# Performance work log

Hardware: AMD Instinct MI355X
Metric: run time of the kernel (lower is better)

Reference implementation:

```python
import jax, jax.numpy as jnp
import numpy as np
import math

N_EMBD = 768
N_HEAD = 12
B, T, S = 8, 1024, 257
HEAD_DIM = N_EMBD // N_HEAD


def _ln(x, g, b, eps=1e-5):
    m = jnp.mean(x, axis=-1, keepdims=True)
    v = jnp.mean(jnp.square(x - m), axis=-1, keepdims=True)
    return (x - m) * jax.lax.rsqrt(v + eps) * g + b


def _heads(t, n_head):
    b, s, c = t.shape
    return t.reshape(b, s, n_head, c // n_head).transpose(0, 2, 1, 3)  # (B,H,S,D)


def setup_inputs() -> dict:
    key = jax.random.key(0)
    ks = jax.random.split(key, 12)
    sc = 0.02
    d, h4 = N_EMBD, 4 * N_EMBD
    return {
        "x": jax.random.normal(ks[0], (B, T, d), jnp.float32),
        "encoder_x": jax.random.normal(ks[1], (B, S, d), jnp.float32),
        "ln1_g": jnp.ones((d,), jnp.float32), "ln1_b": jnp.zeros((d,), jnp.float32),
        "ln2_g": jnp.ones((d,), jnp.float32), "ln2_b": jnp.zeros((d,), jnp.float32),
        "ln3_g": jnp.ones((d,), jnp.float32), "ln3_b": jnp.zeros((d,), jnp.float32),
        "attn_w": jax.random.normal(ks[2], (d, 3 * d), jnp.float32) * sc,
        "attn_b": jnp.zeros((3 * d,), jnp.float32),
        "attn_proj_w": jax.random.normal(ks[3], (d, d), jnp.float32) * sc,
        "attn_proj_b": jnp.zeros((d,), jnp.float32),
        "cross_w": jax.random.normal(ks[4], (d, 3 * d), jnp.float32) * sc,
        "cross_b": jnp.zeros((3 * d,), jnp.float32),
        "cross_proj_w": jax.random.normal(ks[5], (d, d), jnp.float32) * sc,
        "cross_proj_b": jnp.zeros((d,), jnp.float32),
        "fc_w": jax.random.normal(ks[6], (d, h4), jnp.float32) * sc,
        "fc_b": jnp.zeros((h4,), jnp.float32),
        "proj_w": jax.random.normal(ks[7], (h4, d), jnp.float32) * sc,
        "proj_b": jnp.zeros((d,), jnp.float32),
    }


def reference(x, encoder_x, ln1_g, ln1_b, ln2_g, ln2_b, ln3_g, ln3_b,
              attn_w, attn_b, attn_proj_w, attn_proj_b,
              cross_w, cross_b, cross_proj_w, cross_proj_b,
              fc_w, fc_b, proj_w, proj_b):
    d = N_EMBD
    scale = 1.0 / math.sqrt(HEAD_DIM)

    # --- causal self-attention ---
    h = _ln(x, ln1_g, ln1_b)
    qkv = h @ attn_w + attn_b
    q, k, v = (_heads(t, N_HEAD) for t in jnp.split(qkv, 3, axis=-1))
    att = jnp.einsum('bhqd,bhkd->bhqk', q, k) * scale
    t = x.shape[1]
    causal = jnp.tril(jnp.ones((t, t), bool))
    att = jnp.where(causal[None, None], att, -jnp.inf)
    att = jax.nn.softmax(att, axis=-1)
    o = jnp.einsum('bhqk,bhkd->bhqd', att, v)
    o = o.transpose(0, 2, 1, 3).reshape(x.shape)
    x = x + o @ attn_proj_w + attn_proj_b

    # --- cross-attention (shared c_attn for q from x, k/v from encoder) ---
    h = _ln(x, ln2_g, ln2_b)
    q = _heads((h @ cross_w + cross_b)[..., :d], N_HEAD)
    ekv = encoder_x @ cross_w + cross_b
    k = _heads(ekv[..., d:2 * d], N_HEAD)
    v = _heads(ekv[..., 2 * d:], N_HEAD)
    att = jax.nn.softmax(jnp.einsum('bhqd,bhkd->bhqk', q, k) * scale, axis=-1)
    o = jnp.einsum('bhqk,bhkd->bhqd', att, v)
    o = o.transpose(0, 2, 1, 3).reshape(x.shape)
    x = x + o @ cross_proj_w + cross_proj_b

    # --- MLP (GELU tanh) ---
    h = _ln(x, ln3_g, ln3_b)
    h = jax.nn.gelu(h @ fc_w + fc_b, approximate=True)
    x = x + h @ proj_w + proj_b
    return x
```

## Files before the change

kernel.cpp:

```cpp
#include <hip/hip_runtime.h>

typedef __bf16 bf16x8 __attribute__((ext_vector_type(8)));
typedef float  f32x4  __attribute__((ext_vector_type(4)));
typedef unsigned short u16;

#define N_EMBD 768
#define T_LEN 1024
#define S_LEN 257
#define S_PAD 320
#define BATCH 8
#define NH 12
#define BH (BATCH*NH)
#define HD 64

__device__ __forceinline__ u16 f2b(float f){
  union{float f; unsigned u;} v; v.f=f;
  unsigned r=(v.u + 0x7fffu + ((v.u>>16)&1u))>>16;
  return (u16)r;
}
__device__ __forceinline__ float b2f(u16 h){
  union{unsigned u; float f;} v; v.u=((unsigned)h)<<16;
  return v.f;
}
__device__ __forceinline__ void gl_lds16(const void* g, void* l){
  __builtin_amdgcn_global_load_lds((const __attribute__((address_space(1))) void*)g,
                                   (__attribute__((address_space(3))) void*)l, 16, 0, 0);
}

template<int C> __device__ __forceinline__ float dpp_mov_f(float x){
  union{float f;int i;} u; u.f=x;
  u.i = __builtin_amdgcn_mov_dpp(u.i, C, 0xf, 0xf, true);
  return u.f;
}
__device__ __forceinline__ float red16_add(float x){
  x = x + dpp_mov_f<0xB1>(x);
  x = x + dpp_mov_f<0x4E>(x);
  x = x + dpp_mov_f<0x141>(x);
  x = x + dpp_mov_f<0x140>(x);
  return x;
}

__global__ void cvt_f32_bf16(const float* __restrict__ in, u16* __restrict__ out, int n4){
  int i = blockIdx.x*256 + threadIdx.x;
  if(i < n4){
    float4 f = *(const float4*)&in[i*4];
    ushort4 u; u.x=f2b(f.x); u.y=f2b(f.y); u.z=f2b(f.z); u.w=f2b(f.w);
    *(ushort4*)&out[i*4] = u;
  }
}

__global__ void transpose_all(const float* __restrict__ s0,const float* __restrict__ s1,
                              const float* __restrict__ s2,const float* __restrict__ s3,
                              const float* __restrict__ s4,const float* __restrict__ s5,
                              u16* __restrict__ d0,u16* __restrict__ d1,
                              u16* __restrict__ d2,u16* __restrict__ d3,
                              u16* __restrict__ d4,u16* __restrict__ d5){
  __shared__ u16 tile[64][68];
  int id=blockIdx.x;
  const float* in; u16* out; int K,N,t;
  if(id<432)      {in=s0;out=d0;K=768;N=2304;t=id;}
  else if(id<864) {in=s1;out=d1;K=768;N=2304;t=id-432;}
  else if(id<1008){in=s2;out=d2;K=768;N=768;t=id-864;}
  else if(id<1152){in=s3;out=d3;K=768;N=768;t=id-1008;}
  else if(id<1728){in=s4;out=d4;K=768;N=3072;t=id-1152;}
  else            {in=s5;out=d5;K=3072;N=768;t=id-1728;}
  int tiles_n=N>>6;
  int k0=(t/tiles_n)<<6, n0=(t%tiles_n)<<6;
  int tr = threadIdx.x>>4;
  int tc = (threadIdx.x&15)*4;
#pragma unroll
  for(int i=0;i<4;i++){
    float4 f = *(const float4*)&in[(size_t)(k0+tr+i*16)*N + n0 + tc];
    tile[tr+i*16][tc+0]=f2b(f.x); tile[tr+i*16][tc+1]=f2b(f.y);
    tile[tr+i*16][tc+2]=f2b(f.z); tile[tr+i*16][tc+3]=f2b(f.w);
  }
  __syncthreads();
#pragma unroll
  for(int i=0;i<4;i++){
    int n = n0+tr+i*16;
    ushort4 u;
    u.x=tile[tc+0][tr+i*16]; u.y=tile[tc+1][tr+i*16];
    u.z=tile[tc+2][tr+i*16]; u.w=tile[tc+3][tr+i*16];
    *(ushort4*)&out[(size_t)n*K + k0 + tc] = u;
  }
}

__global__ void ln_kernel(const float* __restrict__ x, const float* __restrict__ g,
                          const float* __restrict__ bta, u16* __restrict__ out){
  int row  = blockIdx.x*4 + (threadIdx.x>>6);
  int lane = threadIdx.x&63;
  size_t base = (size_t)row*N_EMBD;
  float v[12];
#pragma unroll
  for(int p=0;p<3;p++){
    int col = p*256 + lane*4;
    float4 f = *(const float4*)&x[base+col];
    v[p*4]=f.x; v[p*4+1]=f.y; v[p*4+2]=f.z; v[p*4+3]=f.w;
  }
  float s=0.f, s2=0.f;
#pragma unroll
  for(int i=0;i<12;i++){ s+=v[i]; s2+=v[i]*v[i]; }
#pragma unroll
  for(int off=1; off<64; off<<=1){ s += __shfl_xor(s,off); s2 += __shfl_xor(s2,off); }
  float mean = s*(1.f/N_EMBD);
  float var  = s2*(1.f/N_EMBD) - mean*mean;
  float rstd = rsqrtf(var + 1e-5f);
#pragma unroll
  for(int p=0;p<3;p++){
    int col = p*256 + lane*4;
#pragma unroll
    for(int j=0;j<4;j++){
      out[base+col+j] = f2b((v[p*4+j]-mean)*rstd*g[col+j] + bta[col+j]);
    }
  }
}

enum { M_QKV_SELF=0, M_Q_CROSS=1, M_KV_CROSS=2, M_RESID_F32=3,
       M_RESID_INPLACE=4, M_GELU=5, M_RESID_OUT=6 };

template<int MODE, int BN>
__global__ void gemm_bt(const u16* __restrict__ A, const u16* __restrict__ Wt,
                        const float* __restrict__ bias,
                        void* out0, void* out1, void* out2, const void* resid,
                        int M, int K, int Ntiles){
  constexpr int MI = (BN==128)?4:2;
  __shared__ u16 As[128*64];
  __shared__ u16 Bs[BN*64];
  int tid=threadIdx.x, wave=tid>>6, lane=tid&63;

  int Mtl = gridDim.x / Ntiles;
  int mt, nt;
  if((Mtl&7)==0){
    int xcd=blockIdx.x&7, j=blockIdx.x>>3, bpx=Mtl>>3;
    int band=j/Ntiles; nt=j-band*Ntiles; mt=xcd*bpx+band;
  } else { mt=blockIdx.x/Ntiles; nt=blockIdx.x-mt*Ntiles; }
  int m0=mt*128, n0=nt*BN;

  int wm = (BN==128)? (wave>>1)*64 : wave*32;
  int wn = (BN==128)? (wave&1)*64  : 0;
  int lrow=lane&15, quad=lane>>4;
  f32x4 acc[MI][4];
  f32x4 z = {0.f,0.f,0.f,0.f};
#pragma unroll
  for(int i=0;i<MI;i++)
#pragma unroll
    for(int j=0;j<4;j++) acc[i][j]=z;

  int srow  = wave*8 + (lane>>3);
  int c_src = (lane&7) ^ ((lane>>3)&7);
  int pa = quad ^ (lrow&7);

  for(int k0=0;k0<K;k0+=64){
#pragma unroll
    for(int i=0;i<4;i++){
      int row = i*32 + srow;
      int ga = min(m0+row, M-1);
      gl_lds16(A + (size_t)ga*K + k0 + c_src*8, &As[(i*32+wave*8)*64]);
    }
#pragma unroll
    for(int i=0;i<BN/32;i++){
      int row = i*32 + srow;
      gl_lds16(Wt + (size_t)(n0+row)*K + k0 + c_src*8, &Bs[(i*32+wave*8)*64]);
    }
    __syncthreads();
    bf16x8 af[MI][2], bfr[4][2];
#pragma unroll
    for(int i=0;i<MI;i++){
      const u16* ab=&As[(wm+i*16+lrow)*64];
      af[i][0]=*(const bf16x8*)(ab+pa*8);
      af[i][1]=*(const bf16x8*)(ab+(pa^4)*8);
    }
#pragma unroll
    for(int i=0;i<4;i++){
      const u16* bb=&Bs[(wn+i*16+lrow)*64];
      bfr[i][0]=*(const bf16x8*)(bb+pa*8);
      bfr[i][1]=*(const bf16x8*)(bb+(pa^4)*8);
    }
#pragma unroll
    for(int h=0;h<2;h++)
#pragma unroll
      for(int mi=0;mi<MI;mi++)
#pragma unroll
        for(int ni=0;ni<4;ni++)
          acc[mi][ni] = __builtin_amdgcn_mfma_f32_16x16x32_bf16(af[mi][h], bfr[ni][h], acc[mi][ni], 0,0,0);
    __syncthreads();
  }

#pragma unroll
  for(int ni=0;ni<4;ni++){
    int n = n0 + wn + ni*16 + lrow;
    float bv = bias[n];
#pragma unroll
    for(int mi=0;mi<MI;mi++){
      int mbase = m0 + wm + mi*16 + quad*4;
      float cr[4];
#pragma unroll
      for(int r=0;r<4;r++) cr[r]=acc[mi][ni][r]+bv;

      if constexpr (MODE==M_QKV_SELF){
        int part=n/768, nn=n-part*768;
        int hh=nn>>6, dd=nn&63;
        int b=mbase>>10, t0=mbase&1023;
        size_t bh=(size_t)(b*NH+hh);
        if(part==0){
#pragma unroll
          for(int r=0;r<4;r++) ((u16*)out0)[(bh*T_LEN+t0+r)*HD+dd]=f2b(cr[r]*0.125f);
        } else if(part==1){
#pragma unroll
          for(int r=0;r<4;r++) ((u16*)out1)[(bh*T_LEN+t0+r)*HD+dd]=f2b(cr[r]);
        } else {
          ushort4 pk; pk.x=f2b(cr[0]); pk.y=f2b(cr[1]); pk.z=f2b(cr[2]); pk.w=f2b(cr[3]);
          *(ushort4*)&((u16*)out2)[(bh*HD+dd)*T_LEN+t0]=pk;
        }
      } else if constexpr (MODE==M_Q_CROSS){
        int b=mbase>>10, t0=mbase&1023;
        int hh=n>>6, dd=n&63;
        size_t bh=(size_t)(b*NH+hh);
#pragma unroll
        for(int r=0;r<4;r++) ((u16*)out0)[(bh*T_LEN+t0+r)*HD+dd]=f2b(cr[r]*0.125f);
      } else if constexpr (MODE==M_KV_CROSS){
        int part=n/768, nn=n-part*768;
        int hh=nn>>6, dd=nn&63;
#pragma unroll
        for(int r=0;r<4;r++){
          int m=mbase+r;
          if(m<M){
            int b=m/S_LEN, s=m-b*S_LEN;
            size_t bh=(size_t)(b*NH+hh);
            if(part==0) ((u16*)out0)[(bh*S_PAD+s)*HD+dd]=f2b(cr[r]);
            else        ((u16*)out1)[(bh*HD+dd)*S_PAD+s]=f2b(cr[r]);
          }
        }
      } else if constexpr (MODE==M_RESID_F32){
        const float* x=(const float*)resid;
#pragma unroll
        for(int r=0;r<4;r++){ int m=mbase+r;
          ((float*)out0)[(size_t)m*768+n]=x[(size_t)m*768+n]+cr[r]; }
      } else if constexpr (MODE==M_RESID_INPLACE){
#pragma unroll
        for(int r=0;r<4;r++){ int m=mbase+r;
          ((float*)out0)[(size_t)m*768+n]+=cr[r]; }
      } else if constexpr (MODE==M_GELU){
#pragma unroll
        for(int r=0;r<4;r++){
          int m=mbase+r;
          float uu=cr[r];
          float zz=0.7978845608028654f*(uu+0.044715f*uu*uu*uu);
          float t=__expf(2.f*zz);
          float th=1.f-2.f/(t+1.f);
          ((u16*)out0)[(size_t)m*3072+n]=f2b(0.5f*uu*(1.f+th));
        }
      } else {
        const float* x=(const float*)resid;
#pragma unroll
        for(int r=0;r<4;r++){ int m=mbase+r;
          ((float*)out0)[(size_t)m*768+n]=x[(size_t)m*768+n]+cr[r]; }
      }
    }
  }
}

template<bool CAUSAL>
__global__ __launch_bounds__(256,2)
void flash_attn(const u16* __restrict__ Q, const u16* __restrict__ Kk,
                const u16* __restrict__ V, u16* __restrict__ O,
                int Skey, int Spad){
  __shared__ u16 KT[2][64*64];
  __shared__ u16 VT[2][64*64];
  __shared__ u16 Plds[4][16][72];
  int bh = blockIdx.x % BH;
  int qbi= blockIdx.x / BH;
  int qb = CAUSAL ? (15-qbi) : qbi;
  int b=bh/NH, hh=bh-b*NH;
  int wave=threadIdx.x>>6, lane=threadIdx.x&63;
  int lrow=lane&15, quad=lane>>4;
  const u16* Qp=Q+(size_t)bh*T_LEN*HD;
  const u16* Kp=Kk+(size_t)bh*Spad*HD;
  const u16* Vp=V+(size_t)bh*HD*Spad;
  u16* Op=O+(size_t)b*T_LEN*N_EMBD+hh*HD;
  int q0 = qb*64 + wave*16;

  int r0    = wave*8 + (lane>>3);
  int c_src = (lane&7) ^ ((lane>>3)&7);

  bf16x8 aq0=*(const bf16x8*)&Qp[(size_t)(q0+lrow)*HD + quad*8];
  bf16x8 aq1=*(const bf16x8*)&Qp[(size_t)(q0+lrow)*HD + 32 + quad*8];

  f32x4 oacc[4];
  f32x4 z={0.f,0.f,0.f,0.f};
#pragma unroll
  for(int i=0;i<4;i++) oacc[i]=z;
  float lsum[4]={0.f,0.f,0.f,0.f};

  int nt = CAUSAL ? (qb+1) : ((Skey+63)>>6);

  {
    gl_lds16(Kp + (size_t)r0*HD        + c_src*8, &KT[0][(wave*8)*64]);
    gl_lds16(Kp + (size_t)(r0+32)*HD   + c_src*8, &KT[0][(32+wave*8)*64]);
    gl_lds16(Vp + (size_t)r0*Spad      + c_src*8, &VT[0][(wave*8)*64]);
    gl_lds16(Vp + (size_t)(r0+32)*Spad + c_src*8, &VT[0][(32+wave*8)*64]);
  }
  __syncthreads();

  int p0 = quad ^ (lrow&7);

  for(int it=0; it<nt; it++){
    int bb = it&1;
    int kt = it*64;
    if(it+1<nt){
      int ktn=(it+1)*64;
      gl_lds16(Kp + (size_t)(ktn+r0)*HD      + c_src*8, &KT[bb^1][(wave*8)*64]);
      gl_lds16(Kp + (size_t)(ktn+r0+32)*HD   + c_src*8, &KT[bb^1][(32+wave*8)*64]);
      gl_lds16(Vp + (size_t)r0*Spad      + ktn + c_src*8, &VT[bb^1][(wave*8)*64]);
      gl_lds16(Vp + (size_t)(r0+32)*Spad + ktn + c_src*8, &VT[bb^1][(32+wave*8)*64]);
    }
    f32x4 s[4];
#pragma unroll
    for(int g=0;g<4;g++){
      const u16* kb=&KT[bb][(g*16+lrow)*64];
      bf16x8 bk0=*(const bf16x8*)(kb+p0*8);
      bf16x8 bk1=*(const bf16x8*)(kb+(p0^4)*8);
      s[g]=z;
      s[g]=__builtin_amdgcn_mfma_f32_16x16x32_bf16(aq0,bk0,s[g],0,0,0);
      s[g]=__builtin_amdgcn_mfma_f32_16x16x32_bf16(aq1,bk1,s[g],0,0,0);
    }
    bool domask = (it==nt-1);
#pragma unroll
    for(int r=0;r<4;r++){
      float sv0=s[0][r], sv1=s[1][r], sv2=s[2][r], sv3=s[3][r];
      if(domask){
        if(CAUSAL){
          int q=q0+quad*4+r;
          if(kt+lrow    >q) sv0=-3.0e38f;
          if(kt+16+lrow >q) sv1=-3.0e38f;
          if(kt+32+lrow >q) sv2=-3.0e38f;
          if(kt+48+lrow >q) sv3=-3.0e38f;
        } else {
          if(kt+lrow    >=Skey) sv0=-3.0e38f;
          if(kt+16+lrow >=Skey) sv1=-3.0e38f;
          if(kt+32+lrow >=Skey) sv2=-3.0e38f;
          if(kt+48+lrow >=Skey) sv3=-3.0e38f;
        }
      }
      float p0e=__expf(sv0), p1e=__expf(sv1);
      float p2e=__expf(sv2), p3e=__expf(sv3);
      lsum[r] += (p0e+p1e)+(p2e+p3e);
      Plds[wave][quad*4+r][lrow]    = f2b(p0e);
      Plds[wave][quad*4+r][16+lrow] = f2b(p1e);
      Plds[wave][quad*4+r][32+lrow] = f2b(p2e);
      Plds[wave][quad*4+r][48+lrow] = f2b(p3e);
    }
    bf16x8 ap0=*(const bf16x8*)&Plds[wave][lrow][quad*8];
    bf16x8 ap1=*(const bf16x8*)&Plds[wave][lrow][32+quad*8];
#pragma unroll
    for(int dt=0;dt<4;dt++){
      const u16* vb=&VT[bb][(dt*16+lrow)*64];
      bf16x8 bv0=*(const bf16x8*)(vb+p0*8);
      bf16x8 bv1=*(const bf16x8*)(vb+(p0^4)*8);
      oacc[dt]=__builtin_amdgcn_mfma_f32_16x16x32_bf16(ap0,bv0,oacc[dt],0,0,0);
      oacc[dt]=__builtin_amdgcn_mfma_f32_16x16x32_bf16(ap1,bv1,oacc[dt],0,0,0);
    }
    __syncthreads();
  }
  float linv[4];
#pragma unroll
  for(int r=0;r<4;r++) linv[r]=1.f/red16_add(lsum[r]);
#pragma unroll
  for(int dt=0;dt<4;dt++){
#pragma unroll
    for(int r=0;r<4;r++){
      int q=q0+quad*4+r;
      Op[(size_t)q*N_EMBD + dt*16 + lrow]=f2b(oacc[dt][r]*linv[r]);
    }
  }
}

extern "C" void kernel_launch(void* const* d_in, const int* in_sizes, int n_in,
                              void* d_out, int out_size, void* d_ws, size_t ws_size,
                              hipStream_t stream){
  const float* x_in   =(const float*)d_in[0];
  const float* enc    =(const float*)d_in[1];
  const float* ln1_g  =(const float*)d_in[2];
  const float* ln1_b  =(const float*)d_in[3];
  const float* ln2_g  =(const float*)d_in[4];
  const float* ln2_b  =(const float*)d_in[5];
  const float* ln3_g  =(const float*)d_in[6];
  const float* ln3_b  =(const float*)d_in[7];
  const float* attn_w =(const float*)d_in[8];
  const float* attn_b =(const float*)d_in[9];
  const float* attn_pw=(const float*)d_in[10];
  const float* attn_pb=(const float*)d_in[11];
  const float* cross_w=(const float*)d_in[12];
  const float* cross_b=(const float*)d_in[13];
  const float* cross_pw=(const float*)d_in[14];
  const float* cross_pb=(const float*)d_in[15];
  const float* fc_w   =(const float*)d_in[16];
  const float* fc_b   =(const float*)d_in[17];
  const float* proj_w =(const float*)d_in[18];
  const float* proj_b =(const float*)d_in[19];

  char* ws=(char*)d_ws;
  u16*  attn_wT  =(u16*)(ws + 0);
  u16*  cross_wT =(u16*)(ws + 3538944);
  u16*  attn_pwT =(u16*)(ws + 7077888);
  u16*  cross_pwT=(u16*)(ws + 8257536);
  u16*  fc_wT    =(u16*)(ws + 9437184);
  u16*  proj_wT  =(u16*)(ws + 14155776);
  float* xcur    =(float*)(ws + 18874368);
  u16*  hbuf     =(u16*)(ws + 44040192);
  u16*  Qs       =(u16*)(ws + 56623104);
  u16*  Ks       =(u16*)(ws + 69206016);
  u16*  Vst      =(u16*)(ws + 81788928);
  u16*  Qc       =(u16*)(ws + 94371840);
  u16*  hf       =(u16*)(ws + 56623104);
  u16*  Kc       =(u16*)(ws + 106954752);
  u16*  Vct      =(u16*)(ws + 110886912);
  u16*  enc_bf   =(u16*)(ws + 114819072);

  dim3 blk(256);
  cvt_f32_bf16<<<1542,blk,0,stream>>>(enc, enc_bf, 394752);
  transpose_all<<<2304,blk,0,stream>>>(attn_w, cross_w, attn_pw, cross_pw, fc_w, proj_w,
                                       attn_wT, cross_wT, attn_pwT, cross_pwT, fc_wT, proj_wT);

  ln_kernel<<<2048,blk,0,stream>>>(x_in, ln1_g, ln1_b, hbuf);
  gemm_bt<M_QKV_SELF,128><<<1152,blk,0,stream>>>(hbuf, attn_wT, attn_b,
      Qs, Ks, Vst, nullptr, 8192, 768, 18);
  flash_attn<true><<<1536,blk,0,stream>>>(Qs, Ks, Vst, hbuf, 1024, 1024);
  gemm_bt<M_RESID_F32,64><<<768,blk,0,stream>>>(hbuf, attn_pwT, attn_pb,
      xcur, nullptr, nullptr, x_in, 8192, 768, 12);

  ln_kernel<<<2048,blk,0,stream>>>(xcur, ln2_g, ln2_b, hbuf);
  gemm_bt<M_Q_CROSS,64><<<768,blk,0,stream>>>(hbuf, cross_wT, cross_b,
      Qc, nullptr, nullptr, nullptr, 8192, 768, 12);
  gemm_bt<M_KV_CROSS,64><<<408,blk,0,stream>>>(enc_bf, cross_wT + 768*768,
      cross_b + 768, Kc, Vct, nullptr, nullptr, 2056, 768, 24);
  flash_attn<false><<<1536,blk,0,stream>>>(Qc, Kc, Vct, hbuf, S_LEN, S_PAD);
  gemm_bt<M_RESID_INPLACE,64><<<768,blk,0,stream>>>(hbuf, cross_pwT, cross_pb,
      xcur, nullptr, nullptr, nullptr, 8192, 768, 12);

  ln_kernel<<<2048,blk,0,stream>>>(xcur, ln3_g, ln3_b, hbuf);
  gemm_bt<M_GELU,128><<<1536,blk,0,stream>>>(hbuf, fc_wT, fc_b,
      hf, nullptr, nullptr, nullptr, 8192, 768, 24);
  gemm_bt<M_RESID_OUT,64><<<768,blk,0,stream>>>(hf, proj_wT, proj_b,
      d_out, nullptr, nullptr, xcur, 8192, 3072, 12);
}
```

Measured before the change: 436.8 us.

## Add 256x256-tile 8-wave GEMM for QKV and FC projections

Introduces a new GEMM kernel with 256x256 output tiles, 512 threads, and double-buffered LDS staging. The A and B half-tiles are loaded in an interleaved, ping-pong schedule, with s_setprio around the MFMA blocks and XCD-aware tile mapping. It replaces the 128-tile GEMM for the self-attention QKV projection and the MLP fc+GELU projection. The aim is more data reuse per block and better overlap of global loads with MFMA work. In exchange, grids are smaller (288 and 384 blocks, so a partial wave on 256 CUs), register pressure is high, and there are many barriers.

```diff
diff --git a/kernel.cpp b/kernel.cpp
--- a/kernel.cpp
+++ b/kernel.cpp
@@ -258,6 +258,193 @@
       }
     }
   }
+}
+
+template<int MODE>
+__global__ __launch_bounds__(512)
+void gemm256(const u16* __restrict__ A, const u16* __restrict__ Wt,
+             const float* __restrict__ bias,
+             void* out0, void* out1, void* out2,
+             int K, int Ntl){
+  __shared__ u16 Asl[2][256*64];
+  __shared__ u16 Bsl[2][256*64];
+  int tid=threadIdx.x, wave=tid>>6, lane=tid&63;
+  int wr=wave>>2, wn=wave&3;
+  int lrow=lane&15, quad=lane>>4;
+
+  int Mtl = gridDim.x / Ntl;
+  int mt, ntb;
+  if((Mtl&7)==0){
+    int xcd=blockIdx.x&7, j=blockIdx.x>>3, bpx=Mtl>>3;
+    int band=j/Ntl; ntb=j-band*Ntl; mt=xcd*bpx+band;
+  } else { mt=blockIdx.x/Ntl; ntb=blockIdx.x-mt*Ntl; }
+  int m0=mt*256, n0=ntb*256;
+
+  int srow8  = lane>>3;
+  int scsrc  = (lane&7) ^ (srow8&7);
+  int pa     = quad ^ (lrow&7);
+
+  float bv[4];
+#pragma unroll
+  for(int ni=0;ni<4;ni++) bv[ni]=bias[n0 + wn*64 + ni*16 + lrow];
+
+  f32x4 acc[8][4];
+  f32x4 z={0.f,0.f,0.f,0.f};
+#pragma unroll
+  for(int i=0;i<8;i++)
+#pragma unroll
+    for(int j=0;j<4;j++) acc[i][j]=z;
+
+  const int NT = K>>6;
+
+#define STG(mat, baser, u, half, lsl) do{                                     \
+    const u16* _g = (mat) + ((size_t)((baser)+(half)*128))*(size_t)K + (size_t)(u)*64; \
+    u16* _l = &lsl[(u)&1][(half)*128*64];                                     \
+    _Pragma("unroll")                                                         \
+    for(int _j=0;_j<2;_j++){                                                  \
+      int _rr = _j*64 + wave*8 + srow8;                                       \
+      gl_lds16(_g + (size_t)_rr*K + scsrc*8, _l + (_j*64+wave*8)*64);         \
+    }                                                                         \
+  }while(0)
+#define MEMFENCE() asm volatile("" ::: "memory")
+#define BAR() __builtin_amdgcn_s_barrier()
+
+  STG(A,  m0, 0, 0, Asl); STG(A,  m0, 0, 1, Asl);
+  STG(Wt, n0, 0, 0, Bsl); STG(Wt, n0, 0, 1, Bsl);
+  STG(A,  m0, 1, 0, Asl); STG(A,  m0, 1, 1, Asl);
+  asm volatile("s_waitcnt vmcnt(4)" ::: "memory");
+  BAR();
+  MEMFENCE();
+
+  bf16x8 a[8][2], b[4][2];
+
+  for(int t=0;t<NT;t++){
+    int s=t&1;
+    const u16* as=&Asl[s][0];
+    const u16* bs=&Bsl[s][0];
+
+#pragma unroll
+    for(int mi=0;mi<4;mi++){
+      const u16* p=&as[(wr*128+mi*16+lrow)*64];
+      a[mi][0]=*(const bf16x8*)(p+pa*8);
+      a[mi][1]=*(const bf16x8*)(p+(pa^4)*8);
+    }
+#pragma unroll
+    for(int ni=0;ni<2;ni++){
+      const u16* p=&bs[(wn*64+ni*16+lrow)*64];
+      b[ni][0]=*(const bf16x8*)(p+pa*8);
+      b[ni][1]=*(const bf16x8*)(p+(pa^4)*8);
+    }
+    if(t+1<NT) STG(Wt, n0, t+1, 0, Bsl);
+    MEMFENCE(); BAR(); MEMFENCE();
+    __builtin_amdgcn_s_setprio(1);
+#pragma unroll
+    for(int mi=0;mi<4;mi++)
+#pragma unroll
+      for(int ni=0;ni<2;ni++){
+        acc[mi][ni]=__builtin_amdgcn_mfma_f32_16x16x32_bf16(a[mi][0],b[ni][0],acc[mi][ni],0,0,0);
+        acc[mi][ni]=__builtin_amdgcn_mfma_f32_16x16x32_bf16(a[mi][1],b[ni][1],acc[mi][ni],0,0,0);
+      }
+    __builtin_amdgcn_s_setprio(0);
+    MEMFENCE(); BAR(); MEMFENCE();
+
+#pragma unroll
+    for(int mi=4;mi<8;mi++){
+      const u16* p=&as[(wr*128+mi*16+lrow)*64];
+      a[mi][0]=*(const bf16x8*)(p+pa*8);
+      a[mi][1]=*(const bf16x8*)(p+(pa^4)*8);
+    }
+    if(t+1<NT) STG(Wt, n0, t+1, 1, Bsl);
+    MEMFENCE(); BAR(); MEMFENCE();
+    __builtin_amdgcn_s_setprio(1);
+#pragma unroll
+    for(int mi=4;mi<8;mi++)
+#pragma unroll
+      for(int ni=0;ni<2;ni++){
+        acc[mi][ni]=__builtin_amdgcn_mfma_f32_16x16x32_bf16(a[mi][0],b[ni][0],acc[mi][ni],0,0,0);
+        acc[mi][ni]=__builtin_amdgcn_mfma_f32_16x16x32_bf16(a[mi][1],b[ni][1],acc[mi][ni],0,0,0);
+      }
+    __builtin_amdgcn_s_setprio(0);
+    MEMFENCE(); BAR(); MEMFENCE();
+
+#pragma unroll
+    for(int ni=2;ni<4;ni++){
+      const u16* p=&bs[(wn*64+ni*16+lrow)*64];
+      b[ni][0]=*(const bf16x8*)(p+pa*8);
+      b[ni][1]=*(const bf16x8*)(p+(pa^4)*8);
+    }
+    if(t+2<NT) STG(A, m0, t+2, 0, Asl);
+    MEMFENCE(); BAR(); MEMFENCE();
+    __builtin_amdgcn_s_setprio(1);
+#pragma unroll
+    for(int mi=0;mi<4;mi++)
+#pragma unroll
+      for(int ni=2;ni<4;ni++){
+        acc[mi][ni]=__builtin_amdgcn_mfma_f32_16x16x32_bf16(a[mi][0],b[ni][0],acc[mi][ni],0,0,0);
+        acc[mi][ni]=__builtin_amdgcn_mfma_f32_16x16x32_bf16(a[mi][1],b[ni][1],acc[mi][ni],0,0,0);
+      }
+    __builtin_amdgcn_s_setprio(0);
+    MEMFENCE(); BAR(); MEMFENCE();
+
+    if(t+2<NT) STG(A, m0, t+2, 1, Asl);
+    MEMFENCE(); BAR(); MEMFENCE();
+    __builtin_amdgcn_s_setprio(1);
+#pragma unroll
+    for(int mi=4;mi<8;mi++)
+#pragma unroll
+      for(int ni=2;ni<4;ni++){
+        acc[mi][ni]=__builtin_amdgcn_mfma_f32_16x16x32_bf16(a[mi][0],b[ni][0],acc[mi][ni],0,0,0);
+        acc[mi][ni]=__builtin_amdgcn_mfma_f32_16x16x32_bf16(a[mi][1],b[ni][1],acc[mi][ni],0,0,0);
+      }
+    __builtin_amdgcn_s_setprio(0);
+    if(t+2<NT){
+      asm volatile("s_waitcnt vmcnt(4)" ::: "memory");
+    } else if(t+1<NT){
+      asm volatile("s_waitcnt vmcnt(0)" ::: "memory");
+    }
+    MEMFENCE(); BAR(); MEMFENCE();
+  }
+#undef STG
+
+#pragma unroll
+  for(int ni=0;ni<4;ni++){
+    int n = n0 + wn*64 + ni*16 + lrow;
+#pragma unroll
+    for(int mi=0;mi<8;mi++){
+      int mbase = m0 + wr*128 + mi*16 + quad*4;
+      float cr[4];
+#pragma unroll
+      for(int r=0;r<4;r++) cr[r]=acc[mi][ni][r]+bv[ni];
+
+      if constexpr (MODE==M_QKV_SELF){
+        int part=n/768, nn=n-part*768;
+        int hh=nn>>6, dd=nn&63;
+        int b_=mbase>>10, t0=mbase&1023;
+        size_t bh=(size_t)(b_*NH+hh);
+        if(part==0){
+#pragma unroll
+          for(int r=0;r<4;r++) ((u16*)out0)[(bh*T_LEN+t0+r)*HD+dd]=f2b(cr[r]*0.125f);
+        } else if(part==1){
+#pragma unroll
+          for(int r=0;r<4;r++) ((u16*)out1)[(bh*T_LEN+t0+r)*HD+dd]=f2b(cr[r]);
+        } else {
+          ushort4 pk; pk.x=f2b(cr[0]); pk.y=f2b(cr[1]); pk.z=f2b(cr[2]); pk.w=f2b(cr[3]);
+          *(ushort4*)&((u16*)out2)[(bh*HD+dd)*T_LEN+t0]=pk;
+        }
+      } else if constexpr (MODE==M_GELU){
+#pragma unroll
+        for(int r=0;r<4;r++){
+          int m=mbase+r;
+          float uu=cr[r];
+          float zz=0.7978845608028654f*(uu+0.044715f*uu*uu*uu);
+          float tt=__expf(2.f*zz);
+          float th=1.f-2.f/(tt+1.f);
+          ((u16*)out0)[(size_t)m*3072+n]=f2b(0.5f*uu*(1.f+th));
+        }
+      }
+    }
+  }
+  (void)out1; (void)out2;
 }
 
 template<bool CAUSAL>
@@ -423,8 +610,8 @@
                                        attn_wT, cross_wT, attn_pwT, cross_pwT, fc_wT, proj_wT);
 
   ln_kernel<<<2048,blk,0,stream>>>(x_in, ln1_g, ln1_b, hbuf);
-  gemm_bt<M_QKV_SELF,128><<<1152,blk,0,stream>>>(hbuf, attn_wT, attn_b,
-      Qs, Ks, Vst, nullptr, 8192, 768, 18);
+  gemm256<M_QKV_SELF><<<288,dim3(512),0,stream>>>(hbuf, attn_wT, attn_b,
+      Qs, Ks, Vst, 768, 9);
   flash_attn<true><<<1536,blk,0,stream>>>(Qs, Ks, Vst, hbuf, 1024, 1024);
   gemm_bt<M_RESID_F32,64><<<768,blk,0,stream>>>(hbuf, attn_pwT, attn_pb,
       xcur, nullptr, nullptr, x_in, 8192, 768, 12);
@@ -439,8 +626,8 @@
       xcur, nullptr, nullptr, nullptr, 8192, 768, 12);
 
   ln_kernel<<<2048,blk,0,stream>>>(xcur, ln3_g, ln3_b, hbuf);
-  gemm_bt<M_GELU,128><<<1536,blk,0,stream>>>(hbuf, fc_wT, fc_b,
-      hf, nullptr, nullptr, nullptr, 8192, 768, 24);
+  gemm256<M_GELU><<<384,dim3(512),0,stream>>>(hbuf, fc_wT, fc_b,
+      hf, nullptr, nullptr, 768, 12);
   gemm_bt<M_RESID_OUT,64><<<768,blk,0,stream>>>(hf, proj_wT, proj_b,
       d_out, nullptr, nullptr, xcur, 8192, 3072, 12);
 }
```

Measured after the change: 486.4 us. +11.4%, slower.

## Double-buffer GEMM LDS tiles and widen N-tiles for projection GEMMs

Applied to the files above, without the earlier changes.

Shared-memory tiles in the GEMM kernel are now double-buffered, so the global-to-LDS copy for the next K-step is issued before the MFMA work on the current buffer. This removes one barrier per step and lets memory loads overlap with matrix math. The projection, cross-Q and output GEMMs also switch from 64-wide to 128-wide N tiles, halving grid size and increasing reuse of the A tile. The cost is twice the LDS per block and fewer blocks, which can lower occupancy and leave the 256 CUs less evenly loaded with 384 blocks.

```diff
diff --git a/kernel.cpp b/kernel.cpp
--- a/kernel.cpp
+++ b/kernel.cpp
@@ -118,14 +118,51 @@
 enum { M_QKV_SELF=0, M_Q_CROSS=1, M_KV_CROSS=2, M_RESID_F32=3,
        M_RESID_INPLACE=4, M_GELU=5, M_RESID_OUT=6 };
 
+#define GB_STAGE(k0v, BUF) do{                                                \
+    _Pragma("unroll")                                                         \
+    for(int i_=0;i_<4;i_++){                                                  \
+      int row_=i_*32+srow;                                                    \
+      int ga_=min(m0+row_, M-1);                                              \
+      gl_lds16(A + (size_t)ga_*K + (k0v) + c_src*8, &As[BUF][(i_*32+wave*8)*64]); \
+    }                                                                         \
+    _Pragma("unroll")                                                         \
+    for(int i_=0;i_<BN/32;i_++){                                              \
+      int row_=i_*32+srow;                                                    \
+      gl_lds16(Wt + (size_t)(n0+row_)*K + (k0v) + c_src*8, &Bs[BUF][(i_*32+wave*8)*64]); \
+    }                                                                         \
+  }while(0)
+
+#define GB_COMPUTE(BUF) do{                                                   \
+    bf16x8 af[MI][2], bfr[4][2];                                              \
+    _Pragma("unroll")                                                         \
+    for(int i_=0;i_<MI;i_++){                                                 \
+      const u16* ab_=&As[BUF][(wm+i_*16+lrow)*64];                            \
+      af[i_][0]=*(const bf16x8*)(ab_+pa*8);                                   \
+      af[i_][1]=*(const bf16x8*)(ab_+(pa^4)*8);                               \
+    }                                                                         \
+    _Pragma("unroll")                                                         \
+    for(int i_=0;i_<4;i_++){                                                  \
+      const u16* bb_=&Bs[BUF][(wn+i_*16+lrow)*64];                            \
+      bfr[i_][0]=*(const bf16x8*)(bb_+pa*8);                                  \
+      bfr[i_][1]=*(const bf16x8*)(bb_+(pa^4)*8);                              \
+    }                                                                         \
+    _Pragma("unroll")                                                         \
+    for(int h_=0;h_<2;h_++)                                                   \
+      _Pragma("unroll")                                                       \
+      for(int mi_=0;mi_<MI;mi_++)                                             \
+        _Pragma("unroll")                                                     \
+        for(int ni_=0;ni_<4;ni_++)                                            \
+          acc[mi_][ni_]=__builtin_amdgcn_mfma_f32_16x16x32_bf16(af[mi_][h_],bfr[ni_][h_],acc[mi_][ni_],0,0,0); \
+  }while(0)
+
 template<int MODE, int BN>
 __global__ void gemm_bt(const u16* __restrict__ A, const u16* __restrict__ Wt,
                         const float* __restrict__ bias,
                         void* out0, void* out1, void* out2, const void* resid,
                         int M, int K, int Ntiles){
   constexpr int MI = (BN==128)?4:2;
-  __shared__ u16 As[128*64];
-  __shared__ u16 Bs[BN*64];
+  __shared__ u16 As[2][128*64];
+  __shared__ u16 Bs[2][BN*64];
   int tid=threadIdx.x, wave=tid>>6, lane=tid&63;
 
   int Mtl = gridDim.x / Ntiles;
@@ -150,40 +187,21 @@
   int c_src = (lane&7) ^ ((lane>>3)&7);
   int pa = quad ^ (lrow&7);
 
-  for(int k0=0;k0<K;k0+=64){
-#pragma unroll
-    for(int i=0;i<4;i++){
-      int row = i*32 + srow;
-      int ga = min(m0+row, M-1);
-      gl_lds16(A + (size_t)ga*K + k0 + c_src*8, &As[(i*32+wave*8)*64]);
-    }
-#pragma unroll
-    for(int i=0;i<BN/32;i++){
-      int row = i*32 + srow;
-      gl_lds16(Wt + (size_t)(n0+row)*K + k0 + c_src*8, &Bs[(i*32+wave*8)*64]);
-    }
+  const int NT = K>>6;
+  GB_STAGE(0, 0);
+  __syncthreads();
+
+  for(int t=0;t<NT;t+=2){
+    if(t+1<NT) GB_STAGE((t+1)*64, 1);
+    __builtin_amdgcn_sched_barrier(0);
+    GB_COMPUTE(0);
     __syncthreads();
-    bf16x8 af[MI][2], bfr[4][2];
-#pragma unroll
-    for(int i=0;i<MI;i++){
-      const u16* ab=&As[(wm+i*16+lrow)*64];
-      af[i][0]=*(const bf16x8*)(ab+pa*8);
-      af[i][1]=*(const bf16x8*)(ab+(pa^4)*8);
-    }
-#pragma unroll
-    for(int i=0;i<4;i++){
-      const u16* bb=&Bs[(wn+i*16+lrow)*64];
-      bfr[i][0]=*(const bf16x8*)(bb+pa*8);
-      bfr[i][1]=*(const bf16x8*)(bb+(pa^4)*8);
-    }
-#pragma unroll
-    for(int h=0;h<2;h++)
-#pragma unroll
-      for(int mi=0;mi<MI;mi++)
-#pragma unroll
-        for(int ni=0;ni<4;ni++)
-          acc[mi][ni] = __builtin_amdgcn_mfma_f32_16x16x32_bf16(af[mi][h], bfr[ni][h], acc[mi][ni], 0,0,0);
-    __syncthreads();
+    if(t+1<NT){
+      if(t+2<NT) GB_STAGE((t+2)*64, 0);
+      __builtin_amdgcn_sched_barrier(0);
+      GB_COMPUTE(1);
+      __syncthreads();
+    }
   }
 
 #pragma unroll
@@ -426,21 +444,21 @@
   gemm_bt<M_QKV_SELF,128><<<1152,blk,0,stream>>>(hbuf, attn_wT, attn_b,
       Qs, Ks, Vst, nullptr, 8192, 768, 18);
   flash_attn<true><<<1536,blk,0,stream>>>(Qs, Ks, Vst, hbuf, 1024, 1024);
-  gemm_bt<M_RESID_F32,64><<<768,blk,0,stream>>>(hbuf, attn_pwT, attn_pb,
-      xcur, nullptr, nullptr, x_in, 8192, 768, 12);
+  gemm_bt<M_RESID_F32,128><<<384,blk,0,stream>>>(hbuf, attn_pwT, attn_pb,
+      xcur, nullptr, nullptr, x_in, 8192, 768, 6);
 
   ln_kernel<<<2048,blk,0,stream>>>(xcur, ln2_g, ln2_b, hbuf);
-  gemm_bt<M_Q_CROSS,64><<<768,blk,0,stream>>>(hbuf, cross_wT, cross_b,
-      Qc, nullptr, nullptr, nullptr, 8192, 768, 12);
+  gemm_bt<M_Q_CROSS,128><<<384,blk,0,stream>>>(hbuf, cross_wT, cross_b,
+      Qc, nullptr, nullptr, nullptr, 8192, 768, 6);
   gemm_bt<M_KV_CROSS,64><<<408,blk,0,stream>>>(enc_bf, cross_wT + 768*768,
       cross_b + 768, Kc, Vct, nullptr, nullptr, 2056, 768, 24);
   flash_attn<false><<<1536,blk,0,stream>>>(Qc, Kc, Vct, hbuf, S_LEN, S_PAD);
-  gemm_bt<M_RESID_INPLACE,64><<<768,blk,0,stream>>>(hbuf, cross_pwT, cross_pb,
-      xcur, nullptr, nullptr, nullptr, 8192, 768, 12);
+  gemm_bt<M_RESID_INPLACE,128><<<384,blk,0,stream>>>(hbuf, cross_pwT, cross_pb,
+      xcur, nullptr, nullptr, nullptr, 8192, 768, 6);
 
   ln_kernel<<<2048,blk,0,stream>>>(xcur, ln3_g, ln3_b, hbuf);
   gemm_bt<M_GELU,128><<<1536,blk,0,stream>>>(hbuf, fc_wT, fc_b,
       hf, nullptr, nullptr, nullptr, 8192, 768, 24);
-  gemm_bt<M_RESID_OUT,64><<<768,blk,0,stream>>>(hf, proj_wT, proj_b,
-      d_out, nullptr, nullptr, xcur, 8192, 3072, 12);
-}
+  gemm_bt<M_RESID_OUT,128><<<384,blk,0,stream>>>(hf, proj_wT, proj_b,
+      d_out, nullptr, nullptr, xcur, 8192, 3072, 6);
+}
```

After: 472.3 us. 1.08x slower.
